# Performance work log

Measured on AMD Instinct MI355X. Metric: run time of the kernel, lower is better.

## Reference

```python
import jax, jax.numpy as jnp
import numpy as np

N = 100000
DIM = 128
N_EDGES = 3200000
EPS = 1e-5


def setup_inputs() -> dict:
    key = jax.random.key(0)
    k1, k2, k3, k4, k5, k6 = jax.random.split(key, 6)
    x = jax.random.normal(k1, (N, DIM), dtype=jnp.float32)
    edge_row = jnp.sort(jax.random.randint(k2, (N_EDGES,), 0, N, dtype=jnp.int64))
    edge_col = jax.random.randint(k3, (N_EDGES,), 0, N, dtype=jnp.int64)
    edge_val = jax.random.uniform(k4, (N_EDGES,), dtype=jnp.float32)
    gamma = jnp.ones((DIM,), dtype=jnp.float32)
    beta = jnp.zeros((DIM,), dtype=jnp.float32)
    return {"x": x, "edge_row": edge_row, "edge_col": edge_col,
            "edge_val": edge_val, "gamma": gamma, "beta": beta}


def _layernorm(h, gamma, beta):
    mu = jnp.mean(h, axis=-1, keepdims=True)
    var = jnp.mean(jnp.square(h - mu), axis=-1, keepdims=True)
    return (h - mu) * jax.lax.rsqrt(var + EPS) * gamma + beta


def reference(x, edge_row, edge_col, edge_val, gamma, beta):
    # sparse adj @ x  ==  segment-sum of val * x[src] into dst rows
    msgs = edge_val[:, None] * x[edge_col]            # [E, DIM]
    h = jax.ops.segment_sum(msgs, edge_row, num_segments=N)  # [N, DIM]
    return _layernorm(h + x, gamma, beta)
```

## Files before the change

### kernel.cpp

```cpp
#include <hip/hip_runtime.h>
#include <hip/hip_fp16.h>

#define DIM 128
#define EPS 1e-5f
#define WAVES_PER_BLOCK 4
#define UNROLL 16

__global__ void prep_kernel(const float4* __restrict__ x4,
                            __half2* __restrict__ xh2,
                            const int* __restrict__ edge_row,
                            int* __restrict__ row_ptr,
                            int n4, int n_nodes, int n_edges)
{
    int i = blockIdx.x * blockDim.x + threadIdx.x;
    if (i < n4) {
        float4 v = x4[i];
        xh2[2 * i]     = __float22half2_rn(make_float2(v.x, v.y));
        xh2[2 * i + 1] = __float22half2_rn(make_float2(v.z, v.w));
    }
    if (i < n_edges) {
        int cur  = edge_row[i];
        int prev = (i == 0) ? -1 : edge_row[i - 1];
        for (int r = prev + 1; r <= cur; ++r) row_ptr[r] = i;
        if (i == n_edges - 1) {
            for (int r = cur + 1; r <= n_nodes; ++r) row_ptr[r] = n_edges;
        }
    }
}

__global__ __launch_bounds__(WAVES_PER_BLOCK * 64)
void gnn_fused_kernel(const __half2* __restrict__ xh2,
                      const int*   __restrict__ row_ptr,
                      const int*   __restrict__ edge_col,
                      const float* __restrict__ edge_val,
                      const float* __restrict__ gamma,
                      const float* __restrict__ beta,
                      float*       __restrict__ out,
                      int n_nodes, int n_edges)
{
    const int wave = threadIdx.x >> 6;
    const int lane = threadIdx.x & 63;
    const int node = blockIdx.x * WAVES_PER_BLOCK + wave;
    if (node >= n_nodes) return;

    const int start = row_ptr[node];
    const int end   = row_ptr[node + 1];
    const unsigned len = (unsigned)(end - start);

    float accx = 0.f, accy = 0.f;

    const int ebase = start & ~3;
    for (int e0 = ebase; e0 < end; e0 += UNROLL) {
        int   c[UNROLL];
        float w[UNROLL];
#pragma unroll
        for (int u4 = 0; u4 < UNROLL / 4; ++u4) {
            int b  = e0 + 4 * u4;
            int bb = (b < n_edges) ? b : 0;
            int4   c4 = *(const int4*)  (edge_col + bb);
            float4 w4 = *(const float4*)(edge_val + bb);
            c[4 * u4 + 0] = c4.x; c[4 * u4 + 1] = c4.y;
            c[4 * u4 + 2] = c4.z; c[4 * u4 + 3] = c4.w;
            w[4 * u4 + 0] = w4.x; w[4 * u4 + 1] = w4.y;
            w[4 * u4 + 2] = w4.z; w[4 * u4 + 3] = w4.w;
        }
#pragma unroll
        for (int u = 0; u < UNROLL; ++u) {
            bool in = (unsigned)(e0 + u - start) < len;
            c[u] = in ? c[u] : 0;
            w[u] = in ? w[u] : 0.f;
        }
        __half2 v[UNROLL];
#pragma unroll
        for (int u = 0; u < UNROLL; ++u)
            v[u] = xh2[c[u] * (DIM / 2) + lane];
#pragma unroll
        for (int u = 0; u < UNROLL; ++u) {
            float2 f = __half22float2(v[u]);
            accx = fmaf(w[u], f.x, accx);
            accy = fmaf(w[u], f.y, accy);
        }
    }

    const float2 xv = __half22float2(xh2[node * (DIM / 2) + lane]);
    const float h0 = accx + xv.x;
    const float h1 = accy + xv.y;

    float s  = h0 + h1;
    float sq = h0 * h0 + h1 * h1;
#pragma unroll
    for (int off = 32; off > 0; off >>= 1) {
        s  += __shfl_xor(s,  off, 64);
        sq += __shfl_xor(sq, off, 64);
    }
    const float mean = s * (1.0f / (float)DIM);
    const float var  = sq * (1.0f / (float)DIM) - mean * mean;
    const float rs   = rsqrtf(var + EPS);

    const float2 g = ((const float2*)gamma)[lane];
    const float2 b = ((const float2*)beta)[lane];
    float2 o;
    o.x = (h0 - mean) * rs * g.x + b.x;
    o.y = (h1 - mean) * rs * g.y + b.y;
    ((float2*)out)[node * (DIM / 2) + lane] = o;
}

extern "C" void kernel_launch(void* const* d_in, const int* in_sizes, int n_in,
                              void* d_out, int out_size, void* d_ws, size_t ws_size,
                              hipStream_t stream)
{
    const float* x        = (const float*)d_in[0];
    const int*   edge_row = (const int*)  d_in[1];
    const int*   edge_col = (const int*)  d_in[2];
    const float* edge_val = (const float*)d_in[3];
    const float* gamma    = (const float*)d_in[4];
    const float* beta     = (const float*)d_in[5];
    float*       out      = (float*)d_out;

    const int n_nodes = in_sizes[0] / DIM;
    const int n_edges = in_sizes[1];
    const int n_elem  = in_sizes[0];
    const int n4      = n_elem / 4;

    __half2* xh2     = (__half2*)d_ws;
    int*     row_ptr = (int*)((char*)d_ws + (size_t)n_elem * sizeof(__half));

    int prep_threads = (n4 > n_edges) ? n4 : n_edges;
    prep_kernel<<<(prep_threads + 255) / 256, 256, 0, stream>>>(
        (const float4*)x, xh2, edge_row, row_ptr, n4, n_nodes, n_edges);

    const int blocks = (n_nodes + WAVES_PER_BLOCK - 1) / WAVES_PER_BLOCK;
    gnn_fused_kernel<<<blocks, WAVES_PER_BLOCK * 64, 0, stream>>>(
        xh2, row_ptr, edge_col, edge_val, gamma, beta, out, n_nodes, n_edges);
}
```

Measured before the change: 249.8 us.

## Gather rows with 16-byte loads, four edges per wave in parallel

Each wave is split into four 16-lane groups. Each group handles a different edge and loads a full 256-byte fp16 row using uint4 (16-byte) loads, instead of every lane loading one half2 per edge. The partial sums are combined across groups with cross-lane shuffles before the layernorm, and the output lanes are remapped so every lane writes two features. This cuts the number of memory instructions per gathered row and should improve gather efficiency. In exchange it adds eight accumulators per lane, extra shuffles, and a less contiguous output write pattern.

Result: faster. 235.7 us (-5.7%).

```diff
diff --git a/kernel.cpp b/kernel.cpp
--- a/kernel.cpp
+++ b/kernel.cpp
@@ -3,8 +3,8 @@
 
 #define DIM 128
 #define EPS 1e-5f
-#define WAVES_PER_BLOCK 4
-#define UNROLL 16
+#define WPB 4
+#define UF  4
 
 __global__ void prep_kernel(const float4* __restrict__ x4,
                             __half2* __restrict__ xh2,
@@ -28,8 +28,8 @@
     }
 }
 
-__global__ __launch_bounds__(WAVES_PER_BLOCK * 64)
-void gnn_fused_kernel(const __half2* __restrict__ xh2,
+__global__ __launch_bounds__(WPB * 64)
+void gnn_fused_kernel(const uint4* __restrict__ xh16,
                       const int*   __restrict__ row_ptr,
                       const int*   __restrict__ edge_col,
                       const float* __restrict__ edge_val,
@@ -40,56 +40,70 @@
 {
     const int wave = threadIdx.x >> 6;
     const int lane = threadIdx.x & 63;
-    const int node = blockIdx.x * WAVES_PER_BLOCK + wave;
+    const int q    = lane >> 4;
+    const int sub  = lane & 15;
+    const int node = blockIdx.x * WPB + wave;
     if (node >= n_nodes) return;
 
     const int start = row_ptr[node];
     const int end   = row_ptr[node + 1];
     const unsigned len = (unsigned)(end - start);
 
-    float accx = 0.f, accy = 0.f;
+    float acc[8];
+#pragma unroll
+    for (int k = 0; k < 8; ++k) acc[k] = 0.f;
 
     const int ebase = start & ~3;
-    for (int e0 = ebase; e0 < end; e0 += UNROLL) {
-        int   c[UNROLL];
-        float w[UNROLL];
+    for (int e0 = ebase; e0 < end; e0 += 4 * UF) {
+        int   c[UF];
+        float w[UF];
 #pragma unroll
-        for (int u4 = 0; u4 < UNROLL / 4; ++u4) {
-            int b  = e0 + 4 * u4;
-            int bb = (b < n_edges) ? b : 0;
-            int4   c4 = *(const int4*)  (edge_col + bb);
-            float4 w4 = *(const float4*)(edge_val + bb);
-            c[4 * u4 + 0] = c4.x; c[4 * u4 + 1] = c4.y;
-            c[4 * u4 + 2] = c4.z; c[4 * u4 + 3] = c4.w;
-            w[4 * u4 + 0] = w4.x; w[4 * u4 + 1] = w4.y;
-            w[4 * u4 + 2] = w4.z; w[4 * u4 + 3] = w4.w;
+        for (int u = 0; u < UF; ++u) {
+            int ei = e0 + 4 * u + q;
+            int eb = min(ei, n_edges - 1);
+            bool in = (unsigned)(ei - start) < len;
+            int   cc = edge_col[eb];
+            float ww = edge_val[eb];
+            c[u] = in ? cc : 0;
+            w[u] = in ? ww : 0.f;
         }
+        uint4 v[UF];
 #pragma unroll
-        for (int u = 0; u < UNROLL; ++u) {
-            bool in = (unsigned)(e0 + u - start) < len;
-            c[u] = in ? c[u] : 0;
-            w[u] = in ? w[u] : 0.f;
-        }
-        __half2 v[UNROLL];
+        for (int u = 0; u < UF; ++u)
+            v[u] = xh16[c[u] * (DIM / 8) + sub];
 #pragma unroll
-        for (int u = 0; u < UNROLL; ++u)
-            v[u] = xh2[c[u] * (DIM / 2) + lane];
+        for (int u = 0; u < UF; ++u) {
+            const __half2* hp = (const __half2*)&v[u];
 #pragma unroll
-        for (int u = 0; u < UNROLL; ++u) {
-            float2 f = __half22float2(v[u]);
-            accx = fmaf(w[u], f.x, accx);
-            accy = fmaf(w[u], f.y, accy);
+            for (int j = 0; j < 4; ++j) {
+                float2 f = __half22float2(hp[j]);
+                acc[2 * j]     = fmaf(w[u], f.x, acc[2 * j]);
+                acc[2 * j + 1] = fmaf(w[u], f.y, acc[2 * j + 1]);
+            }
         }
     }
 
-    const float2 xv = __half22float2(xh2[node * (DIM / 2) + lane]);
-    const float h0 = accx + xv.x;
-    const float h1 = accy + xv.y;
+#pragma unroll
+    for (int k = 0; k < 8; ++k) {
+        acc[k] += __shfl_xor(acc[k], 16, 64);
+        acc[k] += __shfl_xor(acc[k], 32, 64);
+    }
 
-    float s  = h0 + h1;
-    float sq = h0 * h0 + h1 * h1;
+    uint4 xv = xh16[node * (DIM / 8) + sub];
+    const __half2* xp = (const __half2*)&xv;
+    float h[8];
 #pragma unroll
-    for (int off = 32; off > 0; off >>= 1) {
+    for (int j = 0; j < 4; ++j) {
+        float2 f = __half22float2(xp[j]);
+        h[2 * j]     = acc[2 * j]     + f.x;
+        h[2 * j + 1] = acc[2 * j + 1] + f.y;
+    }
+
+    float s = 0.f, sq = 0.f;
+#pragma unroll
+    for (int k = 0; k < 8; ++k) { s += h[k]; sq += h[k] * h[k]; }
+#pragma unroll
+    for (int off = 1; off <= 8; off <<= 1) {
         s  += __shfl_xor(s,  off, 64);
         sq += __shfl_xor(sq, off, 64);
     }
@@ -97,12 +111,15 @@
     const float var  = sq * (1.0f / (float)DIM) - mean * mean;
     const float rs   = rsqrtf(var + EPS);
 
-    const float2 g = ((const float2*)gamma)[lane];
-    const float2 b = ((const float2*)beta)[lane];
+    float hx = (q < 2) ? ((q == 0) ? h[0] : h[2]) : ((q == 2) ? h[4] : h[6]);
+    float hy = (q < 2) ? ((q == 0) ? h[1] : h[3]) : ((q == 2) ? h[5] : h[7]);
+    const int didx = sub * 4 + q;
+    const float2 g = ((const float2*)gamma)[didx];
+    const float2 b = ((const float2*)beta)[didx];
     float2 o;
-    o.x = (h0 - mean) * rs * g.x + b.x;
-    o.y = (h1 - mean) * rs * g.y + b.y;
-    ((float2*)out)[node * (DIM / 2) + lane] = o;
+    o.x = (hx - mean) * rs * g.x + b.x;
+    o.y = (hy - mean) * rs * g.y + b.y;
+    ((float2*)out)[node * (DIM / 2) + didx] = o;
 }
 
 extern "C" void kernel_launch(void* const* d_in, const int* in_sizes, int n_in,
@@ -129,7 +146,8 @@
     prep_kernel<<<(prep_threads + 255) / 256, 256, 0, stream>>>(
         (const float4*)x, xh2, edge_row, row_ptr, n4, n_nodes, n_edges);
 
-    const int blocks = (n_nodes + WAVES_PER_BLOCK - 1) / WAVES_PER_BLOCK;
-    gnn_fused_kernel<<<blocks, WAVES_PER_BLOCK * 64, 0, stream>>>(
-        xh2, row_ptr, edge_col, edge_val, gamma, beta, out, n_nodes, n_edges);
+    const int blocks = (n_nodes + WPB - 1) / WPB;
+    gnn_fused_kernel<<<blocks, WPB * 64, 0, stream>>>(
+        (const uint4*)d_ws, row_ptr, edge_col, edge_val, gamma, beta, out,
+        n_nodes, n_edges);
 }
```
